# Optimization experiments

Hardware: AMD Instinct MI355X
Metric: run time of the kernel (lower is better)

Reference implementation:

```python
import jax, jax.numpy as jnp
import numpy as np

TS = 1.5          # hard-coded sampling period in forward()
W_CENTER = 337.927  # hard-coded center frequency in forward()


def shg_mat(yta):
    """Vectorized createSHGmat: yta is a complex64 vector of length N.
    Row m: Ts * fftshift(fft(fftshift(yta * roll(yta, delay[m]) * shiftFactor))).
    torch.roll(x, s)[j] == x[(j - s) % N], matching the gather below."""
    N = yta.shape[0]
    delays_f = jnp.arange(-(N // 2), N // 2, dtype=jnp.float32)
    delays_i = jnp.arange(-(N // 2), N // 2, dtype=jnp.int32)
    shift_factor = jnp.exp(-1j * 2.0 * W_CENTER * TS * delays_f).astype(jnp.complex64)  # [N]
    idx = (jnp.arange(N, dtype=jnp.int32)[None, :] - delays_i[:, None]) % N  # [N, N]
    y_shift = yta[idx]                                    # [N(delay), N(elem)]
    prod = yta[None, :] * y_shift * shift_factor[None, :]  # elementwise, [N, N]
    prod = jnp.fft.fftshift(prod, axes=-1)
    mat = TS * jnp.fft.fftshift(jnp.fft.fft(prod, axis=-1), axes=-1)
    return mat  # complex64 [N, N]


def frog_error(Tref, Tmeas):
    """calcFrogError: scalar FROG error between reference and measured traces."""
    mu = jnp.sum(Tmeas @ Tref) / jnp.sum(Tref @ Tref)
    r = jnp.sum((Tmeas - mu * Tref) ** 2)
    norm = jnp.float32(Tmeas.size) * jnp.max(Tmeas) ** 2
    return jnp.sqrt(r / norm)


def setup_inputs() -> dict:
    key = jax.random.key(0)
    k1, k2, k3 = jax.random.split(key, 3)
    B, N = 8, 1024
    prediction = jax.random.normal(k1, (B, 2 * N), dtype=jnp.float32)
    label = jax.random.normal(k2, (B, 2 * N), dtype=jnp.float32)
    spectrogram = jax.random.uniform(k3, (N, N), dtype=jnp.float32)
    return {"prediction": prediction, "label": label, "spectrogram": spectrogram}


def reference(prediction, label, spectrogram):
    B, two_n = prediction.shape
    n = two_n // 2
    pred_analytical = (prediction[:, :n] + 1j * prediction[:, n:]).astype(jnp.complex64)  # [B, N]
    mats = jax.vmap(shg_mat)(pred_analytical)          # [B, N, N] complex64
    Tref = jnp.abs(mats)                               # predicted SHG trace magnitude
    errs = jax.vmap(lambda t: frog_error(t, spectrogram))(Tref)  # [B]
    # loss = (sum over batch of frog_error) / batch_size; masked MSE terms in the
    # original are computed but never added to the returned loss, so they are omitted.
    return jnp.mean(errs)
```

## Files before the change

kernel.cpp:

```cpp
#include <hip/hip_runtime.h>
#include <math.h>

#define N 1024
#define B_ 8
#define T_ 512
#define NREP 4
#define CHUNKS 64

#define OFF_SF      0
#define OFF_TA      2048
#define OFF_TB      4096
#define OFF_ROWSUM  4224
#define ZERO_START  12416
#define OFF_COLSUMM 12416
#define OFF_SUMM2   13440
#define OFF_MAXM    13441
#define OFF_SUMMT   13448
#define OFF_SUMTT   13456
#define OFF_COLT    13464
#define WS_END      (OFF_COLT + B_ * NREP * N)

__device__ __forceinline__ float wave_sum(float v) {
    #pragma unroll
    for (int o = 32; o > 0; o >>= 1) v += __shfl_down(v, o, 64);
    return v;
}
__device__ __forceinline__ float wave_max(float v) {
    #pragma unroll
    for (int o = 32; o > 0; o >>= 1) v = fmaxf(v, __shfl_down(v, o, 64));
    return v;
}

__device__ __forceinline__ void cmul(float& xr, float& xi, float wr, float wi) {
    float r = xr * wr - xi * wi;
    float i = xr * wi + xi * wr;
    xr = r; xi = i;
}

__device__ __forceinline__ void dft4(float& r0, float& i0, float& r1, float& i1,
                                     float& r2, float& i2, float& r3, float& i3) {
    float e0r = r0 + r2, e0i = i0 + i2;
    float e1r = r0 - r2, e1i = i0 - i2;
    float e2r = r1 + r3, e2i = i1 + i3;
    float e3r = r1 - r3, e3i = i1 - i3;
    r0 = e0r + e2r; i0 = e0i + e2i;
    r2 = e0r - e2r; i2 = e0i - e2i;
    r1 = e1r + e3i; i1 = e1i - e3r;
    r3 = e1r - e3i; i3 = e1i + e3r;
}

__device__ __forceinline__ void dft16(float xr[16], float xi[16]) {
    #pragma unroll
    for (int b = 0; b < 4; ++b)
        dft4(xr[b], xi[b], xr[4 + b], xi[4 + b], xr[8 + b], xi[8 + b], xr[12 + b], xi[12 + b]);
    const float C1 = 0.9238795325112867f, S1 = 0.3826834323650898f;
    const float C2 = 0.7071067811865476f;
    cmul(xr[5],  xi[5],   C1, -S1);
    cmul(xr[6],  xi[6],   C2, -C2);
    cmul(xr[7],  xi[7],   S1, -C1);
    cmul(xr[9],  xi[9],   C2, -C2);
    { float t = xr[10]; xr[10] = xi[10]; xi[10] = -t; }
    cmul(xr[11], xi[11], -C2, -C2);
    cmul(xr[13], xi[13],  S1, -C1);
    cmul(xr[14], xi[14], -C2, -C2);
    cmul(xr[15], xi[15], -C1,  S1);
    #pragma unroll
    for (int c = 0; c < 4; ++c)
        dft4(xr[4 * c], xi[4 * c], xr[4 * c + 1], xi[4 * c + 1],
             xr[4 * c + 2], xi[4 * c + 2], xr[4 * c + 3], xi[4 * c + 3]);
}

template<int CTRL>
__device__ __forceinline__ float dppf(float x) {
    return __int_as_float(__builtin_amdgcn_update_dpp(
        0, __float_as_int(x), CTRL, 0xF, 0xF, true));
}
#define DPP_XOR1 0xB1
#define DPP_XOR2 0x4E

__global__ __launch_bounds__(256) void k_prep(float* ws) {
    const int e = blockIdx.x * 256 + threadIdx.x;
    if (e < 1024) {
        double ang = -2.0 * 337.927 * 1.5 * (double)(e - 512);
        double s, c;
        sincos(ang, &s, &c);
        ws[OFF_SF + 2 * e]     = (float)c;
        ws[OFF_SF + 2 * e + 1] = (float)s;
    } else if (e < 2048) {
        int e2 = e - 1024;
        int k1 = e2 >> 6, uu = e2 & 63;
        double ang = -2.0 * M_PI * (double)(uu * k1) / 1024.0;
        double s, c;
        sincos(ang, &s, &c);
        ws[OFF_TA + 2 * e2]     = (float)c;
        ws[OFF_TA + 2 * e2 + 1] = (float)s;
    } else if (e < 2112) {
        int e2 = e - 2048;
        int k2 = e2 >> 2, n3 = e2 & 3;
        double ang = -2.0 * M_PI * (double)(n3 * k2) / 64.0;
        double s, c;
        sincos(ang, &s, &c);
        ws[OFF_TB + 2 * e2]     = (float)c;
        ws[OFF_TB + 2 * e2 + 1] = (float)s;
    }
}

__global__ __attribute__((amdgpu_flat_work_group_size(T_, T_), amdgpu_waves_per_eu(4)))
void k_row(const float* __restrict__ pred,
           const float* __restrict__ M,
           float* __restrict__ ws) {
    __shared__ float2 Y2[N];
    __shared__ float2 TP[8][N];
    __shared__ float  colAcc[N];
    __shared__ float2 TB2[64];
    __shared__ float redf[2][8];
    const int t = threadIdx.x;
    const int cnk = blockIdx.x;
    const int y = blockIdx.y;
    const int wid = t >> 6, u = t & 63;

    if (y == 0) {
        const int r0 = cnk * 16;
        float cs0 = 0.f, cs1 = 0.f, sq = 0.f, mx = 0.f;
        for (int r = 0; r < 16; ++r) {
            const float* row = M + (size_t)(r0 + r) * N;
            float v0 = row[t], v1 = row[t + 512];
            cs0 += v0; cs1 += v1;
            sq += v0 * v0 + v1 * v1;
            mx = fmaxf(mx, fmaxf(v0, v1));
        }
        atomicAdd(&ws[OFF_COLSUMM + t],       cs0);
        atomicAdd(&ws[OFF_COLSUMM + t + 512], cs1);
        sq = wave_sum(sq);
        mx = wave_max(mx);
        if (u == 0) { redf[0][wid] = sq; redf[1][wid] = mx; }
        __syncthreads();
        if (t == 0) {
            float ssq = 0.f, smx = 0.f;
            #pragma unroll
            for (int i = 0; i < 8; ++i) { ssq += redf[0][i]; smx = fmaxf(smx, redf[1][i]); }
            atomicAdd(&ws[OFF_SUMM2], ssq);
            atomicMax((unsigned int*)ws + OFF_MAXM, __float_as_uint(smx));
        }
        return;
    }
    const int b = y - 1;

    {
        const float* pr = pred + (size_t)b * 2 * N;
        float2 re = *(const float2*)(pr + 2 * t);
        float2 im = *(const float2*)(pr + N + 2 * t);
        Y2[2 * t]     = make_float2(re.x, im.x);
        Y2[2 * t + 1] = make_float2(re.y, im.y);
        colAcc[t] = 0.f;
        colAcc[t + 512] = 0.f;
        if (t < 64) TB2[t] = ((const float2*)(ws + OFF_TB))[t];
    }
    __syncthreads();

    const int k1u = u >> 2;
    const int n3 = u & 3;
    const int k3 = ((u & 1) << 1) | ((u >> 1) & 1);
    const int clane = (k1u | (k3 << 8)) ^ 512;
    const bool hi2 = (u & 2) != 0;
    const bool odd = (u & 1) != 0;
    float2* tp = TP[wid];
    const float2* sf2 = (const float2*)(ws + OFF_SF);
    const float2* taT = (const float2*)(ws + OFF_TA);

    float mtl = 0.f, ttl = 0.f;
    const int nrow = (cnk == 0 && wid == 0) ? 2 : 1;

    for (int rr = 0; rr < nrow; ++rr) {
        const int m = (rr == 0) ? (cnk * 8 + wid) : 512;
        const int mm = (N - m) & (N - 1);
        const bool domm = (mm != m);
        const float w = domm ? 2.f : 1.f;
        const float mmw = domm ? 1.f : 0.f;

        float xr[16], xi[16];
        const int sbase = (u - m + 512) & (N - 1);
        #pragma unroll
        for (int n1 = 0; n1 < 16; ++n1) {
            int j = (n1 << 6) + u;
            float2 yj = Y2[j];
            float2 sv = sf2[j];
            int s = (sbase + (n1 << 6)) & (N - 1);
            float2 yb = Y2[s];
            float ar = yj.x * sv.x - yj.y * sv.y;
            float ai = yj.x * sv.y + yj.y * sv.x;
            xr[n1] = ar * yb.x - ai * yb.y;
            xi[n1] = ar * yb.y + ai * yb.x;
        }
        dft16(xr, xi);
        #pragma unroll
        for (int r = 1; r < 16; ++r) {
            int k1 = ((r & 3) << 2) | (r >> 2);
            float2 wv = taT[(k1 << 6) + u];
            cmul(xr[r], xi[r], wv.x, wv.y);
        }

        asm volatile("s_waitcnt lgkmcnt(0)" ::: "memory");
        __builtin_amdgcn_sched_barrier(0);
        #pragma unroll
        for (int r = 0; r < 16; ++r) {
            int k1 = ((r & 3) << 2) | (r >> 2);
            int el = (k1 << 6) | (((k1u ^ k1) & 15) << 2) | n3;
            tp[el] = make_float2(xr[r], xi[r]);
        }
        asm volatile("s_waitcnt lgkmcnt(0)" ::: "memory");
        __builtin_amdgcn_sched_barrier(0);
        #pragma unroll
        for (int n2 = 0; n2 < 16; ++n2) {
            int el = (k1u << 6) | (((n2 ^ k1u) & 15) << 2) | n3;
            float2 v = tp[el];
            xr[n2] = v.x; xi[n2] = v.y;
        }

        dft16(xr, xi);
        #pragma unroll
        for (int r = 1; r < 16; ++r) {
            int k2 = ((r & 3) << 2) | (r >> 2);
            float2 wv = TB2[(k2 << 2) | n3];
            cmul(xr[r], xi[r], wv.x, wv.y);
        }

        const float* Mrow  = M + (size_t)m * N + clane;
        const float* Mrow2 = M + (size_t)mm * N + clane;
        const float w225 = w * 2.25f;
        float rs = 0.f;
        #pragma unroll
        for (int r = 0; r < 16; ++r) {
            int k2 = ((r & 3) << 2) | (r >> 2);
            float ar = xr[r], ai = xi[r];
            float br = dppf<DPP_XOR2>(ar), bi = dppf<DPP_XOR2>(ai);
            float zr = hi2 ? (br - ar) : (ar + br);
            float zi = hi2 ? (bi - ai) : (ai + bi);
            float qr = dppf<DPP_XOR1>(zr), qi = dppf<DPP_XOR1>(zi);
            float Xr = odd ? (qr - (hi2 ? zi : zr)) : (zr + (hi2 ? qi : qr));
            float Xi = odd ? (qi + (hi2 ? zr : -zi)) : (zi + (hi2 ? -qr : qi));
            float mag2 = Xr * Xr + Xi * Xi;
            float v = 1.5f * sqrtf(mag2);
            rs  += v;
            ttl += w225 * mag2;
            float ms = Mrow[k2 << 4] + mmw * Mrow2[k2 << 4];
            mtl += ms * v;
            int cc = clane + (k2 << 4);
            atomicAdd(&colAcc[cc ^ ((cc >> 4) & 16)], w * v);
        }
        rs = wave_sum(rs);
        if (u == 0) {
            ws[OFF_ROWSUM + (size_t)b * N + m] = rs;
            if (domm) ws[OFF_ROWSUM + (size_t)b * N + mm] = rs;
        }
    }

    mtl = wave_sum(mtl);
    ttl = wave_sum(ttl);
    if (u == 0) { redf[0][wid] = mtl; redf[1][wid] = ttl; }
    __syncthreads();
    if (t == 0) {
        float smt = 0.f, stt = 0.f;
        #pragma unroll
        for (int i = 0; i < 8; ++i) { smt += redf[0][i]; stt += redf[1][i]; }
        atomicAdd(&ws[OFF_SUMMT + b], smt);
        atomicAdd(&ws[OFF_SUMTT + b], stt);
    }
    float* colT = ws + OFF_COLT + (size_t)(b * NREP + (cnk & (NREP - 1))) * N;
    {
        int j = t;
        atomicAdd(&colT[j], colAcc[j ^ ((j >> 4) & 16)]);
        j = t + 512;
        atomicAdd(&colT[j], colAcc[j ^ ((j >> 4) & 16)]);
    }
}

__global__ __launch_bounds__(256) void k_final(float* ws, float* out) {
    __shared__ double redn[4], redd[4];
    const int b = blockIdx.x;
    const int t = threadIdx.x;
    const int wid = t >> 6, lane = t & 63;
    const float* rowsum = ws + OFF_ROWSUM + (size_t)b * N;
    double num = 0.0, den = 0.0;
    #pragma unroll
    for (int q = 0; q < 4; ++q) {
        int j = t + 256 * q;
        double r = (double)rowsum[j];
        float ct = 0.f;
        #pragma unroll
        for (int rep = 0; rep < NREP; ++rep)
            ct += ws[OFF_COLT + (size_t)(b * NREP + rep) * N + j];
        num += (double)ws[OFF_COLSUMM + j] * r;
        den += (double)ct * r;
    }
    #pragma unroll
    for (int o = 32; o > 0; o >>= 1) {
        num += __shfl_down(num, o, 64);
        den += __shfl_down(den, o, 64);
    }
    if (lane == 0) { redn[wid] = num; redd[wid] = den; }
    __syncthreads();
    if (t == 0) {
        double NUM = redn[0] + redn[1] + redn[2] + redn[3];
        double DEN = redd[0] + redd[1] + redd[2] + redd[3];
        double mu = NUM / DEN;
        double r = (double)ws[OFF_SUMM2] - 2.0 * mu * (double)ws[OFF_SUMMT + b]
                 + mu * mu * (double)ws[OFF_SUMTT + b];
        float mx = ws[OFF_MAXM];
        double norm = 1048576.0 * (double)mx * (double)mx;
        atomicAdd(out, (float)(sqrt(r / norm) / 8.0));
    }
}

extern "C" void kernel_launch(void* const* d_in, const int* in_sizes, int n_in,
                              void* d_out, int out_size, void* d_ws, size_t ws_size,
                              hipStream_t stream) {
    const float* pred = (const float*)d_in[0];
    const float* M = (const float*)d_in[2];
    float* ws = (float*)d_ws;
    float* out = (float*)d_out;

    hipMemsetAsync(ws + ZERO_START, 0, (size_t)(WS_END - ZERO_START) * sizeof(float), stream);
    hipMemsetAsync(out, 0, sizeof(float), stream);
    k_prep<<<9, 256, 0, stream>>>(ws);
    dim3 grid(CHUNKS, B_ + 1);
    k_row<<<grid, T_, 0, stream>>>(pred, M, ws);
    k_final<<<B_, 256, 0, stream>>>(ws, out);
}
```

Baseline: 119.1 us.

## Stage twiddle tables in LDS and halve per-wave transpose buffer with two-phase exchange

Copies the shift-factor and first-stage twiddle tables from global memory into shared memory once per block, replacing per-element global loads inside the FFT. The per-wave transpose scratch is halved by splitting the exchange into two phases, where half the lanes read after each half of the data is written, so the larger twiddle tables fit in LDS. The waves-per-EU hint is relaxed to a 2-4 range. The cost is extra LDS fill work, additional waitcnt barriers, and divergent lane halves during the transpose.

```diff
diff --git a/kernel.cpp b/kernel.cpp
--- a/kernel.cpp
+++ b/kernel.cpp
@@ -105,15 +105,17 @@
     }
 }
 
-__global__ __attribute__((amdgpu_flat_work_group_size(T_, T_), amdgpu_waves_per_eu(4)))
+__global__ __attribute__((amdgpu_flat_work_group_size(T_, T_), amdgpu_waves_per_eu(2, 4)))
 void k_row(const float* __restrict__ pred,
            const float* __restrict__ M,
            float* __restrict__ ws) {
     __shared__ float2 Y2[N];
-    __shared__ float2 TP[8][N];
+    __shared__ float2 TPh[8][N / 2];
+    __shared__ float2 sfL[N];
+    __shared__ float2 taL[N];
+    __shared__ float2 TB2[64];
     __shared__ float  colAcc[N];
-    __shared__ float2 TB2[64];
-    __shared__ float redf[2][8];
+    __shared__ float  redf[2][8];
     const int t = threadIdx.x;
     const int cnk = blockIdx.x;
     const int y = blockIdx.y;
@@ -152,9 +154,14 @@
         float2 im = *(const float2*)(pr + N + 2 * t);
         Y2[2 * t]     = make_float2(re.x, im.x);
         Y2[2 * t + 1] = make_float2(re.y, im.y);
+        const float2* g = (const float2*)ws;
+        sfL[t]       = g[OFF_SF / 2 + t];
+        sfL[t + 512] = g[OFF_SF / 2 + t + 512];
+        taL[t]       = g[OFF_TA / 2 + t];
+        taL[t + 512] = g[OFF_TA / 2 + t + 512];
+        if (t < 64) TB2[t] = g[OFF_TB / 2 + t];
         colAcc[t] = 0.f;
         colAcc[t + 512] = 0.f;
-        if (t < 64) TB2[t] = ((const float2*)(ws + OFF_TB))[t];
     }
     __syncthreads();
 
@@ -164,9 +171,7 @@
     const int clane = (k1u | (k3 << 8)) ^ 512;
     const bool hi2 = (u & 2) != 0;
     const bool odd = (u & 1) != 0;
-    float2* tp = TP[wid];
-    const float2* sf2 = (const float2*)(ws + OFF_SF);
-    const float2* taT = (const float2*)(ws + OFF_TA);
+    float2* tp = TPh[wid];
 
     float mtl = 0.f, ttl = 0.f;
     const int nrow = (cnk == 0 && wid == 0) ? 2 : 1;
@@ -184,7 +189,7 @@
         for (int n1 = 0; n1 < 16; ++n1) {
             int j = (n1 << 6) + u;
             float2 yj = Y2[j];
-            float2 sv = sf2[j];
+            float2 sv = sfL[j];
             int s = (sbase + (n1 << 6)) & (N - 1);
             float2 yb = Y2[s];
             float ar = yj.x * sv.x - yj.y * sv.y;
@@ -196,33 +201,50 @@
         #pragma unroll
         for (int r = 1; r < 16; ++r) {
             int k1 = ((r & 3) << 2) | (r >> 2);
-            float2 wv = taT[(k1 << 6) + u];
+            float2 wv = taL[(k1 << 6) + u];
             cmul(xr[r], xi[r], wv.x, wv.y);
         }
 
+        float yr[16], yi[16];
         asm volatile("s_waitcnt lgkmcnt(0)" ::: "memory");
-        __builtin_amdgcn_sched_barrier(0);
-        #pragma unroll
-        for (int r = 0; r < 16; ++r) {
+        #pragma unroll
+        for (int r = 0; r < 16; ++r) if ((r & 3) < 2) {
             int k1 = ((r & 3) << 2) | (r >> 2);
-            int el = (k1 << 6) | (((k1u ^ k1) & 15) << 2) | n3;
+            int el = ((k1 & 7) << 6) | (((k1u ^ k1) & 15) << 2) | n3;
             tp[el] = make_float2(xr[r], xi[r]);
         }
         asm volatile("s_waitcnt lgkmcnt(0)" ::: "memory");
-        __builtin_amdgcn_sched_barrier(0);
-        #pragma unroll
-        for (int n2 = 0; n2 < 16; ++n2) {
-            int el = (k1u << 6) | (((n2 ^ k1u) & 15) << 2) | n3;
-            float2 v = tp[el];
-            xr[n2] = v.x; xi[n2] = v.y;
-        }
-
-        dft16(xr, xi);
+        if (u < 32) {
+            #pragma unroll
+            for (int n2 = 0; n2 < 16; ++n2) {
+                int el = ((k1u & 7) << 6) | (((n2 ^ k1u) & 15) << 2) | n3;
+                float2 v = tp[el];
+                yr[n2] = v.x; yi[n2] = v.y;
+            }
+        }
+        asm volatile("s_waitcnt lgkmcnt(0)" ::: "memory");
+        #pragma unroll
+        for (int r = 0; r < 16; ++r) if ((r & 3) >= 2) {
+            int k1 = ((r & 3) << 2) | (r >> 2);
+            int el = ((k1 & 7) << 6) | (((k1u ^ k1) & 15) << 2) | n3;
+            tp[el] = make_float2(xr[r], xi[r]);
+        }
+        asm volatile("s_waitcnt lgkmcnt(0)" ::: "memory");
+        if (u >= 32) {
+            #pragma unroll
+            for (int n2 = 0; n2 < 16; ++n2) {
+                int el = ((k1u & 7) << 6) | (((n2 ^ k1u) & 15) << 2) | n3;
+                float2 v = tp[el];
+                yr[n2] = v.x; yi[n2] = v.y;
+            }
+        }
+
+        dft16(yr, yi);
         #pragma unroll
         for (int r = 1; r < 16; ++r) {
             int k2 = ((r & 3) << 2) | (r >> 2);
             float2 wv = TB2[(k2 << 2) | n3];
-            cmul(xr[r], xi[r], wv.x, wv.y);
+            cmul(yr[r], yi[r], wv.x, wv.y);
         }
 
         const float* Mrow  = M + (size_t)m * N + clane;
@@ -232,7 +254,7 @@
         #pragma unroll
         for (int r = 0; r < 16; ++r) {
             int k2 = ((r & 3) << 2) | (r >> 2);
-            float ar = xr[r], ai = xi[r];
+            float ar = yr[r], ai = yi[r];
             float br = dppf<DPP_XOR2>(ar), bi = dppf<DPP_XOR2>(ai);
             float zr = hi2 ? (br - ar) : (ar + br);
             float zi = hi2 ? (bi - ai) : (ai + bi);
@@ -266,8 +288,8 @@
         atomicAdd(&ws[OFF_SUMMT + b], smt);
         atomicAdd(&ws[OFF_SUMTT + b], stt);
     }
-    float* colT = ws + OFF_COLT + (size_t)(b * NREP + (cnk & (NREP - 1))) * N;
     {
+        float* colT = ws + OFF_COLT + (size_t)(b * NREP + (cnk & (NREP - 1))) * N;
         int j = t;
         atomicAdd(&colT[j], colAcc[j ^ ((j >> 4) & 16)]);
         j = t + 512;
```

Result: faster. 106.0 us (-11.0%).
